# Optimization experiments

Measured on AMD Instinct MI355X. Metric: run time of the kernel, lower is better.

## Reference

```python
import jax, jax.numpy as jnp
import numpy as np
import math

B, L, E, H, FF = 8, 1024, 1024, 16, 4096
DH = E // H  # 64
EPS = 1e-10


def layer_norm(x, gamma, beta):
    mean = jnp.mean(x, axis=-1, keepdims=True)
    var = jnp.mean((x - mean) ** 2, axis=-1, keepdims=True)
    return gamma * (x - mean) / jnp.sqrt(var + EPS) + beta


def setup_inputs() -> dict:
    key = jax.random.key(0)
    ks = jax.random.split(key, 16)
    c_qk = math.sqrt(6.0 / (E + DH))
    c_o = math.sqrt(6.0 / (H * DH + E))
    c1 = math.sqrt(6.0 / (E + FF))
    c2 = math.sqrt(6.0 / (FF + E))
    u = lambda k, shp, c: jax.random.uniform(k, shp, jnp.float32, -c, c)
    return {
        "x": jax.random.normal(ks[0], (B, L, E), jnp.float32),
        # per-head projections stacked: [H, E, DH] (stored input-major = W^T of torch Linear)
        "Wq": u(ks[1], (H, E, DH), c_qk), "bq": jnp.zeros((H, DH), jnp.float32),
        "Wk": u(ks[2], (H, E, DH), c_qk), "bk": jnp.zeros((H, DH), jnp.float32),
        "Wv": u(ks[3], (H, E, DH), c_qk), "bv": jnp.zeros((H, DH), jnp.float32),
        "Wo": u(ks[4], (H * DH, E), c_o), "bo": jnp.zeros((E,), jnp.float32),
        "W1": u(ks[5], (E, FF), c1), "b1": jnp.zeros((FF,), jnp.float32),
        "W2": u(ks[6], (FF, E), c2), "b2": jnp.zeros((E,), jnp.float32),
        "gamma1": jnp.ones((E,), jnp.float32), "beta1": jnp.zeros((E,), jnp.float32),
        "gamma2": jnp.ones((E,), jnp.float32), "beta2": jnp.zeros((E,), jnp.float32),
    }


def reference(x, Wq, bq, Wk, bk, Wv, bv, Wo, bo, W1, b1, W2, b2, gamma1, beta1, gamma2, beta2):
    # multi-head attention (all heads batched; concat order == head order)
    q = jnp.einsum("ble,hed->bhld", x, Wq) + bq[None, :, None, :]
    k = jnp.einsum("ble,hed->bhld", x, Wk) + bk[None, :, None, :]
    v = jnp.einsum("ble,hed->bhld", x, Wv) + bv[None, :, None, :]
    scores = jnp.einsum("bhld,bhmd->bhlm", q, k) / math.sqrt(DH)
    weights = jax.nn.softmax(scores, axis=-1)
    y = jnp.einsum("bhlm,bhmd->bhld", weights, v)          # [B,H,L,DH]
    concat = y.transpose(0, 2, 1, 3).reshape(B, L, H * DH)  # [B,L,E]
    out1 = concat @ Wo + bo
    # residual + LN (dropout p=0 -> identity)
    out2 = layer_norm(out1 + x, gamma1, beta1)
    # FFN
    out3 = jax.nn.relu(out2 @ W1 + b1) @ W2 + b2
    return layer_norm(out3 + out2, gamma2, beta2)
```

## Files before the change

### kernel.cpp

```cpp
#include <hip/hip_runtime.h>
#include <hip/hip_bf16.h>

#define BB 8
#define LL 1024
#define EE 1024
#define HH 16
#define DHH 64
#define FFF 4096

typedef __attribute__((ext_vector_type(8))) short short8;
typedef __attribute__((ext_vector_type(4))) float f32x4;

__device__ inline f32x4 mfma16(short8 a, short8 b, f32x4 c) {
    return __builtin_amdgcn_mfma_f32_16x16x32_bf16(a, b, c, 0, 0, 0);
}

__device__ inline void async_ld16(const __hip_bfloat16* g, __hip_bfloat16* l) {
    __builtin_amdgcn_global_load_lds(
        (const __attribute__((address_space(1))) void*)g,
        (__attribute__((address_space(3))) void*)l, 16, 0, 0);
}

__device__ inline unsigned short bf16bits(float f) {
    __hip_bfloat16 h = __float2bfloat16(f);
    return *reinterpret_cast<unsigned short*>(&h);
}

__device__ inline float bf2f(unsigned short u) {
    unsigned v = ((unsigned)u) << 16;
    return *reinterpret_cast<float*>(&v);
}

__device__ inline float exp2_fast(float x) {
    float r;
    asm("v_exp_f32 %0, %1" : "=v"(r) : "v"(x));
    return r;
}

__device__ inline unsigned cvt_pk_bf16(float lo, float hi) {
    unsigned r;
    asm("v_cvt_pk_bf16_f32 %0, %1, %2" : "=v"(r) : "v"(lo), "v"(hi));
    return r;
}

__device__ inline void wg_barrier() {
    __builtin_amdgcn_sched_barrier(0);
    asm volatile("" ::: "memory");
    __builtin_amdgcn_s_barrier();
    asm volatile("" ::: "memory");
    __builtin_amdgcn_sched_barrier(0);
}

__global__ __launch_bounds__(256) void wtrans_all(
    const float* __restrict__ Wq, const float* __restrict__ Wk, const float* __restrict__ Wv,
    const float* __restrict__ Wo, const float* __restrict__ W1, const float* __restrict__ W2,
    const float* __restrict__ x,
    __hip_bfloat16* __restrict__ wqkvt, __hip_bfloat16* __restrict__ wot,
    __hip_bfloat16* __restrict__ w1t, __hip_bfloat16* __restrict__ w2t,
    __hip_bfloat16* __restrict__ xb) {
    const int id = blockIdx.x;
    const int tid = threadIdx.x;
    if (id >= 3072) {
        const int xi = id - 3072;
#pragma unroll
        for (int j = 0; j < 4; ++j) {
            const size_t f4 = (size_t)xi * 1024 + j * 256 + tid;
            float4 v = reinterpret_cast<const float4*>(x)[f4];
            ushort4 o;
            o.x = bf16bits(v.x); o.y = bf16bits(v.y); o.z = bf16bits(v.z); o.w = bf16bits(v.w);
            reinterpret_cast<ushort4*>(xb)[f4] = o;
        }
        return;
    }
    const float* src;
    __hip_bfloat16* dst;
    int K, N, k0, n0;
    if (id < 768) {
        const int which = id >> 8, r = id & 255;
        const int z = r >> 4, xx = r & 15;
        src = ((which == 0) ? Wq : (which == 1) ? Wk : Wv) + (size_t)z * 65536;
        dst = wqkvt + (size_t)which * 1024 * 1024 + (size_t)z * 65536;
        K = 1024; N = 64; k0 = xx * 64; n0 = 0;
    } else if (id < 1024) {
        const int r = id - 768;
        src = Wo; dst = wot; K = 1024; N = 1024; k0 = (r & 15) * 64; n0 = (r >> 4) * 64;
    } else if (id < 2048) {
        const int r = id - 1024;
        src = W1; dst = w1t; K = 1024; N = 4096; k0 = (r & 15) * 64; n0 = (r >> 4) * 64;
    } else {
        const int r = id - 2048;
        src = W2; dst = w2t; K = 4096; N = 1024; k0 = (r & 63) * 64; n0 = (r >> 6) * 64;
    }
    __shared__ __hip_bfloat16 t[64 * 66];
#pragma unroll
    for (int i = 0; i < 16; ++i) {
        int idx = tid + i * 256;
        int kr = idx >> 6, nc = idx & 63;
        t[kr * 66 + nc] = __float2bfloat16(src[(size_t)(k0 + kr) * N + n0 + nc]);
    }
    __syncthreads();
#pragma unroll
    for (int i = 0; i < 16; ++i) {
        int idx = tid + i * 256;
        int nr = idx >> 6, kc = idx & 63;
        dst[(size_t)(n0 + nr) * K + k0 + kc] = t[kc * 66 + nr];
    }
}

template <int MODE, int CM, int CN, int ZX>
__global__ __launch_bounds__(512, 2) void gemm256(
    const __hip_bfloat16* __restrict__ A, const __hip_bfloat16* __restrict__ Bm,
    int M, int N, int K, int ksplit, size_t zstride, void* __restrict__ Cout,
    const float* __restrict__ bias0, const float* __restrict__ bias1,
    const float* __restrict__ bias2, __hip_bfloat16* __restrict__ vtout) {
    __shared__ __hip_bfloat16 lds[2][2][2][128 * 64];
    const int flat = blockIdx.x + gridDim.x * (blockIdx.y + gridDim.y * blockIdx.z);
    const int xcd = flat & 7, rank = flat >> 3;
    const int mc = xcd & 3, hc = xcd >> 2;
    const int ml = rank / CN, nl = rank % CN;
    const int mb = mc * CM + ml;
    const int nb = ZX ? nl : (hc * CN + nl);
    const int zb = ZX ? hc : 0;
    const int m0 = mb * 256, n0 = nb * 256;
    const int tid = threadIdx.x;
    const int wid = tid >> 6, l = tid & 63;
    const int wm = wid >> 2, wn = wid & 3;
    const int lr = l & 15, lg = l >> 4;
    const int T = K / (64 * ksplit);
    const int kb = zb * T;

    const int c0 = tid, c1 = tid + 512;
    const int r0 = c0 >> 3, s0 = (((c0 & 7) ^ (r0 & 7)) << 3);
    const int r1 = c1 >> 3, s1 = (((c1 & 7) ^ (r1 & 7)) << 3);
    const int ldst0 = wid * 512;
    const int ldst1 = 4096 + wid * 512;

#define STAGE(bi, isb, half, kt)                                                             \
    do {                                                                                     \
        const __hip_bfloat16* _s = (isb) ? Bm : A;                                           \
        const int _br = ((isb) ? n0 : m0) + (half) * 128;                                    \
        __hip_bfloat16* _d = &lds[bi][isb][half][0];                                         \
        async_ld16(_s + (size_t)(_br + r0) * K + (size_t)(kb + (kt)) * 64 + s0, _d + ldst0); \
        async_ld16(_s + (size_t)(_br + r1) * K + (size_t)(kb + (kt)) * 64 + s1, _d + ldst1); \
    } while (0)

    f32x4 acc[8][4];
#pragma unroll
    for (int m = 0; m < 8; ++m)
#pragma unroll
        for (int n = 0; n < 4; ++n) acc[m][n] = (f32x4){0.f, 0.f, 0.f, 0.f};

    short8 aLo[4][2], aHi[4][2], bR[4][2];

#define LDA(dst, bi, m, kh)                                                          \
    do {                                                                             \
        const int _ra = (m) * 16 + lr;                                               \
        const int _sl = ((kh) * 4 + lg) ^ (_ra & 7);                                 \
        dst = *reinterpret_cast<const short8*>(&lds[bi][0][wm][_ra * 64 + _sl * 8]); \
    } while (0)
#define LDB(dst, bi, n, kh)                                                               \
    do {                                                                                  \
        const int _rb = (wn & 1) * 64 + (n) * 16 + lr;                                    \
        const int _sl = ((kh) * 4 + lg) ^ (_rb & 7);                                      \
        dst = *reinterpret_cast<const short8*>(&lds[bi][1][wn >> 1][_rb * 64 + _sl * 8]); \
    } while (0)

#define RD_ALO(bi)                      \
    _Pragma("unroll") for (int m = 0; m < 4; ++m) { \
        LDA(aLo[m][0], bi, m, 0);       \
        LDA(aLo[m][1], bi, m, 1);       \
    }
#define RD_AHI(bi)                      \
    _Pragma("unroll") for (int m = 0; m < 4; ++m) { \
        LDA(aHi[m][0], bi, m + 4, 0);   \
        LDA(aHi[m][1], bi, m + 4, 1);   \
    }
#define RD_B01(bi)                      \
    _Pragma("unroll") for (int n = 0; n < 2; ++n) { \
        LDB(bR[n][0], bi, n, 0);        \
        LDB(bR[n][1], bi, n, 1);        \
    }
#define RD_B23(bi)                      \
    _Pragma("unroll") for (int n = 2; n < 4; ++n) { \
        LDB(bR[n][0], bi, n, 0);        \
        LDB(bR[n][1], bi, n, 1);        \
    }
#define MFMA_Q(mbase, afr, nlo)                                            \
    __builtin_amdgcn_s_setprio(1);                                         \
    _Pragma("unroll") for (int m = 0; m < 4; ++m) {                        \
        _Pragma("unroll") for (int n = (nlo); n < (nlo) + 2; ++n) {        \
            acc[(mbase) + m][n] = mfma16(afr[m][0], bR[n][0], acc[(mbase) + m][n]); \
            acc[(mbase) + m][n] = mfma16(afr[m][1], bR[n][1], acc[(mbase) + m][n]); \
        }                                                                  \
    }                                                                      \
    __builtin_amdgcn_s_setprio(0);

    STAGE(0, 1, 0, 0);
    STAGE(0, 1, 1, 0);
    STAGE(0, 0, 0, 0);
    STAGE(0, 0, 1, 0);
    if (T > 1) {
        STAGE(1, 1, 0, 1);
        STAGE(1, 1, 1, 1);
        STAGE(1, 0, 0, 1);
        STAGE(1, 0, 1, 1);
        asm volatile("s_waitcnt vmcnt(8)" ::: "memory");
    } else {
        asm volatile("s_waitcnt vmcnt(0)" ::: "memory");
    }
    wg_barrier();
    RD_ALO(0);
    RD_B01(0);

    for (int t = 0; t < T; ++t) {
        const int cur = t & 1, nxt = cur ^ 1;
        wg_barrier();
        MFMA_Q(0, aLo, 0);
        RD_B23(cur);
        wg_barrier();
        MFMA_Q(0, aLo, 2);
        RD_AHI(cur);
        if (t + 2 < T) STAGE(cur, 1, 0, t + 2);
        wg_barrier();
        MFMA_Q(4, aHi, 0);
        if (t + 2 < T) {
            asm volatile("s_waitcnt vmcnt(2)" ::: "memory");
            STAGE(cur, 1, 1, t + 2);
            STAGE(cur, 0, 0, t + 2);
            STAGE(cur, 0, 1, t + 2);
        } else if (t + 1 < T) {
            asm volatile("s_waitcnt vmcnt(0)" ::: "memory");
        }
        wg_barrier();
        MFMA_Q(4, aHi, 2);
        if (t + 1 < T) {
            RD_ALO(nxt);
            RD_B01(nxt);
        }
    }
#undef STAGE
#undef LDA
#undef LDB
#undef RD_ALO
#undef RD_AHI
#undef RD_B01
#undef RD_B23
#undef MFMA_Q

    asm volatile("s_waitcnt vmcnt(0)" ::: "memory");
    __syncthreads();

    float* eb = reinterpret_cast<float*>(&lds[0][0][0][0]) + wid * (16 * 68);
    const int erow = l >> 3, ec = l & 7;
    const int rowg = m0 + wm * 128;
    const int colg = n0 + wn * 64;
    float bv[4];
#pragma unroll
    for (int n = 0; n < 4; ++n) {
        if constexpr (MODE == 0) {
            const int col = colg + n * 16 + lr;
            int s = col >> 10;
            const float* bp = (s == 0) ? bias0 : ((s == 1) ? bias1 : bias2);
            bv[n] = bp[col & 1023];
        } else if constexpr (MODE == 2) {
            bv[n] = bias0[colg + n * 16 + lr];
        } else {
            bv[n] = 0.f;
        }
    }
    __hip_bfloat16* Cb = (MODE == 4)
        ? ((__hip_bfloat16*)Cout + (size_t)zb * zstride)
        : (__hip_bfloat16*)Cout;
#pragma unroll
    for (int m = 0; m < 8; ++m) {
#pragma unroll
        for (int n = 0; n < 4; ++n)
#pragma unroll
            for (int r = 0; r < 4; ++r) {
                float v = acc[m][n][r] + bv[n];
                if constexpr (MODE == 2) v = fmaxf(v, 0.f);
                eb[(lg * 4 + r) * 68 + n * 16 + lr] = v;
            }
#pragma unroll
        for (int i = 0; i < 2; ++i) {
            const int rr = erow + i * 8;
            float4 v0 = *reinterpret_cast<float4*>(&eb[rr * 68 + ec * 8]);
            float4 v1 = *reinterpret_cast<float4*>(&eb[rr * 68 + ec * 8 + 4]);
            uint4 o;
            o.x = cvt_pk_bf16(v0.x, v0.y);
            o.y = cvt_pk_bf16(v0.z, v0.w);
            o.z = cvt_pk_bf16(v1.x, v1.y);
            o.w = cvt_pk_bf16(v1.z, v1.w);
            *reinterpret_cast<uint4*>(&Cb[(size_t)(rowg + m * 16 + rr) * N + colg + ec * 8]) = o;
        }
        if constexpr (MODE == 0) {
            if (colg >= 2048) {
                const int h2 = (colg - 2048) >> 6;
                const int bh2 = ((rowg >> 10) << 4) + h2;
                const int l0 = (rowg & 1023) + m * 16;
                uint4 o0, o1;
                o0.x = cvt_pk_bf16(eb[0 * 68 + l], eb[1 * 68 + l]);
                o0.y = cvt_pk_bf16(eb[2 * 68 + l], eb[3 * 68 + l]);
                o0.z = cvt_pk_bf16(eb[4 * 68 + l], eb[5 * 68 + l]);
                o0.w = cvt_pk_bf16(eb[6 * 68 + l], eb[7 * 68 + l]);
                o1.x = cvt_pk_bf16(eb[8 * 68 + l], eb[9 * 68 + l]);
                o1.y = cvt_pk_bf16(eb[10 * 68 + l], eb[11 * 68 + l]);
                o1.z = cvt_pk_bf16(eb[12 * 68 + l], eb[13 * 68 + l]);
                o1.w = cvt_pk_bf16(eb[14 * 68 + l], eb[15 * 68 + l]);
                __hip_bfloat16* vrow = vtout + ((size_t)bh2 * 64 + l) * 1024 + l0;
                *reinterpret_cast<uint4*>(vrow) = o0;
                *reinterpret_cast<uint4*>(vrow + 8) = o1;
            }
        }
    }
}

__global__ __launch_bounds__(512, 4) void attn4(const __hip_bfloat16* __restrict__ qkv,
                                                const __hip_bfloat16* __restrict__ vt,
                                                __hip_bfloat16* __restrict__ cat) {
    const int orig = blockIdx.y * 4 + blockIdx.x;
    const int swz = (orig & 7) * 64 + (orig >> 3);
    const int qt = swz & 3, bh = swz >> 2;
    const int b = bh >> 4, h = bh & 15;
    const int tid = threadIdx.x, w = tid >> 6, l = tid & 63;
    const int lr = l & 15, lg = l >> 4;
    const int sw = lr & 7;

    __shared__ __hip_bfloat16 Ks[2][64 * 64];
    __shared__ __hip_bfloat16 Vs[2][64 * 64];
    __shared__ __hip_bfloat16 plds[8][32 * 72];

    short8 qa[2][2];
#pragma unroll
    for (int q = 0; q < 2; ++q) {
        const size_t qrow = (size_t)(b * LL + qt * 256 + w * 32 + q * 16 + lr);
        qa[q][0] = *reinterpret_cast<const short8*>(qkv + qrow * 3072 + h * 64 + lg * 8);
        qa[q][1] = *reinterpret_cast<const short8*>(qkv + qrow * 3072 + h * 64 + 32 + lg * 8);
    }

    const int rA = tid >> 3, sA = (((tid & 7) ^ (rA & 7)) << 3);
    const __hip_bfloat16* kg = qkv + (size_t)(b * LL + rA) * 3072 + 1024 + h * 64 + sA;
    const __hip_bfloat16* vg = vt + ((size_t)bh * 64 + rA) * LL + sA;

#define STAGE_KV(bi, k0)                                        \
    do {                                                        \
        async_ld16(kg + (size_t)(k0) * 3072, &Ks[bi][w * 512]); \
        async_ld16(vg + (k0), &Vs[bi][w * 512]);                \
    } while (0)

    float mrun[2] = {-INFINITY, -INFINITY}, lrun[2] = {0.f, 0.f};
    f32x4 oacc[2][4];
#pragma unroll
    for (int q = 0; q < 2; ++q)
#pragma unroll
        for (int n = 0; n < 4; ++n) oacc[q][n] = (f32x4){0.f, 0.f, 0.f, 0.f};

    STAGE_KV(0, 0);
    asm volatile("s_waitcnt vmcnt(0)" ::: "memory");
    __syncthreads();

    const float SCALE = 0.18033688011112042f;

    int cur = 0;
    for (int kt = 0; kt < 16; ++kt) {
        if (kt < 15) STAGE_KV(cur ^ 1, (kt + 1) * 64);

        f32x4 s[2][4];
#pragma unroll
        for (int m = 0; m < 4; ++m) {
            const int krow = m * 16 + lr;
            const short8 kf0 =
                *reinterpret_cast<const short8*>(&Ks[cur][krow * 64 + ((lg ^ sw) << 3)]);
            const short8 kf1 =
                *reinterpret_cast<const short8*>(&Ks[cur][krow * 64 + (((lg + 4) ^ sw) << 3)]);
#pragma unroll
            for (int q = 0; q < 2; ++q) {
                f32x4 t = (f32x4){0.f, 0.f, 0.f, 0.f};
                t = mfma16(kf0, qa[q][0], t);
                t = mfma16(kf1, qa[q][1], t);
                s[q][m] = t * SCALE;
            }
        }
        float smax[2];
#pragma unroll
        for (int q = 0; q < 2; ++q) {
            float mx = s[q][0][0];
#pragma unroll
            for (int m = 0; m < 4; ++m)
#pragma unroll
                for (int r = 0; r < 4; ++r) mx = fmaxf(mx, s[q][m][r]);
            mx = fmaxf(mx, __shfl_xor(mx, 16, 64));
            mx = fmaxf(mx, __shfl_xor(mx, 32, 64));
            smax[q] = mx;
        }
        if (__any(fmaxf(smax[0] - mrun[0], smax[1] - mrun[1]) > 8.0f)) {
#pragma unroll
            for (int q = 0; q < 2; ++q) {
                const float mnew = fmaxf(mrun[q], smax[q]);
                const float alpha = exp2_fast(mrun[q] - mnew);
                mrun[q] = mnew;
                lrun[q] *= alpha;
#pragma unroll
                for (int r = 0; r < 4; ++r) {
                    const float aD = __shfl(alpha, lg * 4 + r, 64);
#pragma unroll
                    for (int n = 0; n < 4; ++n) oacc[q][n][r] *= aD;
                }
            }
        }
#pragma unroll
        for (int q = 0; q < 2; ++q) {
            float tsum = 0.f;
#pragma unroll
            for (int m = 0; m < 4; ++m) {
                float p0 = exp2_fast(s[q][m][0] - mrun[q]);
                float p1 = exp2_fast(s[q][m][1] - mrun[q]);
                float p2 = exp2_fast(s[q][m][2] - mrun[q]);
                float p3 = exp2_fast(s[q][m][3] - mrun[q]);
                tsum += (p0 + p1) + (p2 + p3);
                uint2 d;
                d.x = cvt_pk_bf16(p0, p1);
                d.y = cvt_pk_bf16(p2, p3);
                *reinterpret_cast<uint2*>(&plds[w][(q * 16 + lr) * 72 + m * 16 + lg * 4]) = d;
            }
            tsum += __shfl_xor(tsum, 16, 64);
            tsum += __shfl_xor(tsum, 32, 64);
            lrun[q] += tsum;
        }
        asm volatile("s_waitcnt lgkmcnt(0)" ::: "memory");
        __builtin_amdgcn_sched_barrier(0);

        short8 pa[2][2];
#pragma unroll
        for (int q = 0; q < 2; ++q) {
            pa[q][0] = *reinterpret_cast<const short8*>(&plds[w][(q * 16 + lr) * 72 + lg * 8]);
            pa[q][1] =
                *reinterpret_cast<const short8*>(&plds[w][(q * 16 + lr) * 72 + 32 + lg * 8]);
        }
#pragma unroll
        for (int n = 0; n < 4; ++n) {
            const int vrow = n * 16 + lr;
            const short8 vf0 =
                *reinterpret_cast<const short8*>(&Vs[cur][vrow * 64 + ((lg ^ sw) << 3)]);
            const short8 vf1 =
                *reinterpret_cast<const short8*>(&Vs[cur][vrow * 64 + (((lg + 4) ^ sw) << 3)]);
#pragma unroll
            for (int q = 0; q < 2; ++q) {
                oacc[q][n] = mfma16(pa[q][0], vf0, oacc[q][n]);
                oacc[q][n] = mfma16(pa[q][1], vf1, oacc[q][n]);
            }
        }

        asm volatile("s_waitcnt vmcnt(0)" ::: "memory");
        __syncthreads();
        cur ^= 1;
    }
#undef STAGE_KV

#pragma unroll
    for (int q = 0; q < 2; ++q) {
        float rinv[4];
#pragma unroll
        for (int r = 0; r < 4; ++r) rinv[r] = 1.0f / __shfl(lrun[q], lg * 4 + r, 64);
#pragma unroll
        for (int n = 0; n < 4; ++n)
#pragma unroll
            for (int r = 0; r < 4; ++r) {
                const float v = oacc[q][n][r] * rinv[r];
                cat[(size_t)(b * LL + qt * 256 + w * 32 + q * 16 + lg * 4 + r) * EE + h * 64 +
                    n * 16 + lr] = __float2bfloat16(v);
            }
    }
}

template <bool CBF16, bool OUTF32>
__global__ __launch_bounds__(256) void ln_fused(const __hip_bfloat16* __restrict__ a,
                                                const __hip_bfloat16* __restrict__ b,
                                                const void* __restrict__ cv,
                                                const float* __restrict__ colbias,
                                                const float* __restrict__ gamma,
                                                const float* __restrict__ beta,
                                                void* __restrict__ outv) {
    const int row = blockIdx.x, tid = threadIdx.x;
    const size_t base = (size_t)row * EE;
    const ushort4 ua = reinterpret_cast<const ushort4*>(a + base)[tid];
    const ushort4 ub = reinterpret_cast<const ushort4*>(b + base)[tid];
    float4 z;
    if constexpr (CBF16) {
        const ushort4 uc =
            reinterpret_cast<const ushort4*>((const __hip_bfloat16*)cv + base)[tid];
        z.x = bf2f(uc.x); z.y = bf2f(uc.y); z.z = bf2f(uc.z); z.w = bf2f(uc.w);
    } else {
        z = reinterpret_cast<const float4*>((const float*)cv + base)[tid];
    }
    float4 cb = reinterpret_cast<const float4*>(colbias)[tid];
    float4 x;
    x.x = bf2f(ua.x) + bf2f(ub.x) + z.x + cb.x;
    x.y = bf2f(ua.y) + bf2f(ub.y) + z.y + cb.y;
    x.z = bf2f(ua.z) + bf2f(ub.z) + z.z + cb.z;
    x.w = bf2f(ua.w) + bf2f(ub.w) + z.w + cb.w;
    float s = x.x + x.y + x.z + x.w;
    float s2 = x.x * x.x + x.y * x.y + x.z * x.z + x.w * x.w;
#pragma unroll
    for (int msk = 1; msk < 64; msk <<= 1) {
        s += __shfl_xor(s, msk, 64);
        s2 += __shfl_xor(s2, msk, 64);
    }
    __shared__ float red[8];
    const int w = tid >> 6, l = tid & 63;
    if (l == 0) { red[w] = s; red[4 + w] = s2; }
    __syncthreads();
    s = red[0] + red[1] + red[2] + red[3];
    s2 = red[4] + red[5] + red[6] + red[7];
    const float mean = s * (1.f / 1024.f);
    const float var = s2 * (1.f / 1024.f) - mean * mean;
    const float rstd = rsqrtf(var + 1e-10f);
    float4 g = reinterpret_cast<const float4*>(gamma)[tid];
    float4 bt = reinterpret_cast<const float4*>(beta)[tid];
    float4 o;
    o.x = g.x * (x.x - mean) * rstd + bt.x;
    o.y = g.y * (x.y - mean) * rstd + bt.y;
    o.z = g.z * (x.z - mean) * rstd + bt.z;
    o.w = g.w * (x.w - mean) * rstd + bt.w;
    if constexpr (OUTF32) {
        reinterpret_cast<float4*>((float*)outv + base)[tid] = o;
    } else {
        ushort4 ob;
        ob.x = bf16bits(o.x); ob.y = bf16bits(o.y); ob.z = bf16bits(o.z); ob.w = bf16bits(o.w);
        reinterpret_cast<ushort4*>((__hip_bfloat16*)outv + base)[tid] = ob;
    }
}

extern "C" void kernel_launch(void* const* d_in, const int* in_sizes, int n_in,
                              void* d_out, int out_size, void* d_ws, size_t ws_size,
                              hipStream_t stream) {
    const float* x = (const float*)d_in[0];
    const float* Wq = (const float*)d_in[1];
    const float* bq = (const float*)d_in[2];
    const float* Wk = (const float*)d_in[3];
    const float* bk = (const float*)d_in[4];
    const float* Wv = (const float*)d_in[5];
    const float* bv = (const float*)d_in[6];
    const float* Wo = (const float*)d_in[7];
    const float* bo = (const float*)d_in[8];
    const float* W1 = (const float*)d_in[9];
    const float* b1 = (const float*)d_in[10];
    const float* W2 = (const float*)d_in[11];
    const float* b2 = (const float*)d_in[12];
    const float* gamma1 = (const float*)d_in[13];
    const float* beta1 = (const float*)d_in[14];
    const float* gamma2 = (const float*)d_in[15];
    const float* beta2 = (const float*)d_in[16];
    float* out = (float*)d_out;

    char* Wb = (char*)d_ws;
    const size_t MB = (size_t)1 << 20;
    if (ws_size < 168 * MB) return;
    __hip_bfloat16* xb = (__hip_bfloat16*)(Wb + 0 * MB);
    __hip_bfloat16* wqkvt = (__hip_bfloat16*)(Wb + 16 * MB);
    __hip_bfloat16* wot = (__hip_bfloat16*)(Wb + 22 * MB);
    __hip_bfloat16* w1t = (__hip_bfloat16*)(Wb + 24 * MB);
    __hip_bfloat16* w2t = (__hip_bfloat16*)(Wb + 32 * MB);
    __hip_bfloat16* qkvb = (__hip_bfloat16*)(Wb + 40 * MB);
    __hip_bfloat16* vtb = (__hip_bfloat16*)(Wb + 88 * MB);
    __hip_bfloat16* catb = (__hip_bfloat16*)(Wb + 104 * MB);
    __hip_bfloat16* p0 = (__hip_bfloat16*)(Wb + 40 * MB);
    __hip_bfloat16* out2b = (__hip_bfloat16*)(Wb + 136 * MB);
    __hip_bfloat16* hbuf = (__hip_bfloat16*)(Wb + 40 * MB);
    __hip_bfloat16* q0 = (__hip_bfloat16*)(Wb + 0 * MB);
    const size_t PSTRIDE = (size_t)8192 * 1024;

    wtrans_all<<<5120, 256, 0, stream>>>(Wq, Wk, Wv, Wo, W1, W2, x, wqkvt, wot, w1t, w2t, xb);
    gemm256<0, 8, 6, 0><<<dim3(32, 12, 1), 512, 0, stream>>>(xb, wqkvt, 8192, 3072, 1024, 1, 0,
                                                             qkvb, bq, bk, bv, vtb);
    attn4<<<dim3(4, 128), 512, 0, stream>>>(qkvb, vtb, catb);
    gemm256<4, 8, 4, 1><<<dim3(32, 4, 2), 512, 0, stream>>>(catb, wot, 8192, 1024, 1024, 2,
                                                            PSTRIDE, p0, nullptr, nullptr,
                                                            nullptr, nullptr);
    ln_fused<false, false><<<8192, 256, 0, stream>>>(p0, p0 + PSTRIDE, x, bo, gamma1, beta1,
                                                     out2b);
    gemm256<2, 8, 8, 0><<<dim3(32, 16, 1), 512, 0, stream>>>(out2b, w1t, 8192, 4096, 1024, 1, 0,
                                                             hbuf, b1, nullptr, nullptr,
                                                             nullptr);
    gemm256<4, 8, 4, 1><<<dim3(32, 4, 2), 512, 0, stream>>>(hbuf, w2t, 8192, 1024, 4096, 2,
                                                            PSTRIDE, q0, nullptr, nullptr,
                                                            nullptr, nullptr);
    ln_fused<true, true><<<8192, 256, 0, stream>>>(q0, q0 + PSTRIDE, out2b, b2, gamma2, beta2,
                                                   out);
}
```

Measured before the change: 301.5 us.

## Halve GEMM k-tile to 32 and use 4-way split-K for Wo and W2 projections

The GEMM k-step drops from 64 to 32, which halves LDS use per block and simplifies the pipeline to two barriers per iteration with a new swizzled layout. The Wo and W2 GEMMs switch from 2-way to 4-way split-K, giving 512 blocks instead of 256 to fill the CUs. The layer-norm kernels now sum four bf16 partials. The cost is more partial-buffer traffic, more barriers per unit of K, and extra bf16 rounding from summing four partials.

```diff
diff --git a/kernel.cpp b/kernel.cpp
--- a/kernel.cpp
+++ b/kernel.cpp
@@ -107,41 +107,44 @@
     }
 }
 
-template <int MODE, int CM, int CN, int ZX>
+template <int MODE, int CM, int CN, int NZ>
 __global__ __launch_bounds__(512, 2) void gemm256(
     const __hip_bfloat16* __restrict__ A, const __hip_bfloat16* __restrict__ Bm,
-    int M, int N, int K, int ksplit, size_t zstride, void* __restrict__ Cout,
+    int M, int N, int K, size_t zstride, size_t z2off, void* __restrict__ Cout,
     const float* __restrict__ bias0, const float* __restrict__ bias1,
     const float* __restrict__ bias2, __hip_bfloat16* __restrict__ vtout) {
-    __shared__ __hip_bfloat16 lds[2][2][2][128 * 64];
+    __shared__ __hip_bfloat16 lds[2][2][2][64 * 64];
     const int flat = blockIdx.x + gridDim.x * (blockIdx.y + gridDim.y * blockIdx.z);
     const int xcd = flat & 7, rank = flat >> 3;
-    const int mc = xcd & 3, hc = xcd >> 2;
-    const int ml = rank / CN, nl = rank % CN;
-    const int mb = mc * CM + ml;
-    const int nb = ZX ? nl : (hc * CN + nl);
-    const int zb = ZX ? hc : 0;
+    int mb, nb, zb;
+    if constexpr (NZ == 1) {
+        mb = (xcd & 3) * CM + rank / CN;
+        nb = (xcd >> 2) * CN + rank % CN;
+        zb = 0;
+    } else {
+        mb = xcd * CM + rank / (CN * NZ);
+        const int rem = rank % (CN * NZ);
+        zb = rem / CN;
+        nb = rem % CN;
+    }
     const int m0 = mb * 256, n0 = nb * 256;
     const int tid = threadIdx.x;
     const int wid = tid >> 6, l = tid & 63;
     const int wm = wid >> 2, wn = wid & 3;
     const int lr = l & 15, lg = l >> 4;
-    const int T = K / (64 * ksplit);
+    const int T = K / (32 * NZ);
     const int kb = zb * T;
 
-    const int c0 = tid, c1 = tid + 512;
-    const int r0 = c0 >> 3, s0 = (((c0 & 7) ^ (r0 & 7)) << 3);
-    const int r1 = c1 >> 3, s1 = (((c1 & 7) ^ (r1 & 7)) << 3);
-    const int ldst0 = wid * 512;
-    const int ldst1 = 4096 + wid * 512;
-
-#define STAGE(bi, isb, half, kt)                                                             \
-    do {                                                                                     \
-        const __hip_bfloat16* _s = (isb) ? Bm : A;                                           \
-        const int _br = ((isb) ? n0 : m0) + (half) * 128;                                    \
-        __hip_bfloat16* _d = &lds[bi][isb][half][0];                                         \
-        async_ld16(_s + (size_t)(_br + r0) * K + (size_t)(kb + (kt)) * 64 + s0, _d + ldst0); \
-        async_ld16(_s + (size_t)(_br + r1) * K + (size_t)(kb + (kt)) * 64 + s1, _d + ldst1); \
+    const int p_ = tid >> 3, c_ = tid & 7, u_ = c_ ^ (p_ & 7);
+    const int srow = 2 * p_ + (u_ >> 2);
+    const int skc = (u_ & 3) << 3;
+
+#define STAGE(bi, isb, half, kt)                                                     \
+    do {                                                                             \
+        const __hip_bfloat16* _s = (isb) ? Bm : A;                                   \
+        const int _br = ((isb) ? n0 : m0) + (half) * 128;                            \
+        async_ld16(_s + (size_t)(_br + srow) * K + (size_t)(kb + (kt)) * 32 + skc,   \
+                   &lds[bi][isb][half][0] + wid * 512);                              \
     } while (0)
 
     f32x4 acc[8][4];
@@ -150,92 +153,70 @@
 #pragma unroll
         for (int n = 0; n < 4; ++n) acc[m][n] = (f32x4){0.f, 0.f, 0.f, 0.f};
 
-    short8 aLo[4][2], aHi[4][2], bR[4][2];
-
-#define LDA(dst, bi, m, kh)                                                          \
+    short8 aLo[4], aHi[4], bR[4];
+
+#define LDA(dst, bi, m)                                                              \
     do {                                                                             \
-        const int _ra = (m) * 16 + lr;                                               \
-        const int _sl = ((kh) * 4 + lg) ^ (_ra & 7);                                 \
-        dst = *reinterpret_cast<const short8*>(&lds[bi][0][wm][_ra * 64 + _sl * 8]); \
+        const int _r = (m) * 16 + lr;                                                \
+        const int _p = _r >> 1;                                                      \
+        const int _c = (lg + ((_r & 1) << 2)) ^ (_p & 7);                            \
+        dst = *reinterpret_cast<const short8*>(&lds[bi][0][wm][_p * 64 + _c * 8]);   \
     } while (0)
-#define LDB(dst, bi, n, kh)                                                               \
-    do {                                                                                  \
-        const int _rb = (wn & 1) * 64 + (n) * 16 + lr;                                    \
-        const int _sl = ((kh) * 4 + lg) ^ (_rb & 7);                                      \
-        dst = *reinterpret_cast<const short8*>(&lds[bi][1][wn >> 1][_rb * 64 + _sl * 8]); \
+#define LDB(dst, bi, n)                                                              \
+    do {                                                                             \
+        const int _r = (wn & 1) * 64 + (n) * 16 + lr;                                \
+        const int _p = _r >> 1;                                                      \
+        const int _c = (lg + ((_r & 1) << 2)) ^ (_p & 7);                            \
+        dst = *reinterpret_cast<const short8*>(&lds[bi][1][wn >> 1][_p * 64 + _c * 8]); \
     } while (0)
 
-#define RD_ALO(bi)                      \
-    _Pragma("unroll") for (int m = 0; m < 4; ++m) { \
-        LDA(aLo[m][0], bi, m, 0);       \
-        LDA(aLo[m][1], bi, m, 1);       \
-    }
-#define RD_AHI(bi)                      \
-    _Pragma("unroll") for (int m = 0; m < 4; ++m) { \
-        LDA(aHi[m][0], bi, m + 4, 0);   \
-        LDA(aHi[m][1], bi, m + 4, 1);   \
-    }
-#define RD_B01(bi)                      \
-    _Pragma("unroll") for (int n = 0; n < 2; ++n) { \
-        LDB(bR[n][0], bi, n, 0);        \
-        LDB(bR[n][1], bi, n, 1);        \
-    }
-#define RD_B23(bi)                      \
-    _Pragma("unroll") for (int n = 2; n < 4; ++n) { \
-        LDB(bR[n][0], bi, n, 0);        \
-        LDB(bR[n][1], bi, n, 1);        \
-    }
-#define MFMA_Q(mbase, afr, nlo)                                            \
-    __builtin_amdgcn_s_setprio(1);                                         \
-    _Pragma("unroll") for (int m = 0; m < 4; ++m) {                        \
-        _Pragma("unroll") for (int n = (nlo); n < (nlo) + 2; ++n) {        \
-            acc[(mbase) + m][n] = mfma16(afr[m][0], bR[n][0], acc[(mbase) + m][n]); \
-            acc[(mbase) + m][n] = mfma16(afr[m][1], bR[n][1], acc[(mbase) + m][n]); \
-        }                                                                  \
-    }                                                                      \
+#define RD_ALO(bi) \
+    _Pragma("unroll") for (int m = 0; m < 4; ++m) LDA(aLo[m], bi, m);
+#define RD_AHI(bi) \
+    _Pragma("unroll") for (int m = 0; m < 4; ++m) LDA(aHi[m], bi, m + 4);
+#define RD_B(bi) \
+    _Pragma("unroll") for (int n = 0; n < 4; ++n) LDB(bR[n], bi, n);
+#define MFMA_Q(mbase, afr)                                                           \
+    __builtin_amdgcn_s_setprio(1);                                                   \
+    _Pragma("unroll") for (int m = 0; m < 4; ++m) {                                  \
+        _Pragma("unroll") for (int n = 0; n < 4; ++n) {                              \
+            acc[(mbase) + m][n] = mfma16(afr[m], bR[n], acc[(mbase) + m][n]);        \
+        }                                                                            \
+    }                                                                                \
     __builtin_amdgcn_s_setprio(0);
 
     STAGE(0, 1, 0, 0);
     STAGE(0, 1, 1, 0);
     STAGE(0, 0, 0, 0);
     STAGE(0, 0, 1, 0);
-    if (T > 1) {
-        STAGE(1, 1, 0, 1);
-        STAGE(1, 1, 1, 1);
-        STAGE(1, 0, 0, 1);
-        STAGE(1, 0, 1, 1);
-        asm volatile("s_waitcnt vmcnt(8)" ::: "memory");
-    } else {
-        asm volatile("s_waitcnt vmcnt(0)" ::: "memory");
-    }
+    STAGE(1, 1, 0, 1);
+    STAGE(1, 1, 1, 1);
+    STAGE(1, 0, 0, 1);
+    STAGE(1, 0, 1, 1);
+    asm volatile("s_waitcnt vmcnt(4)" ::: "memory");
     wg_barrier();
     RD_ALO(0);
-    RD_B01(0);
+    RD_B(0);
 
     for (int t = 0; t < T; ++t) {
         const int cur = t & 1, nxt = cur ^ 1;
+        MFMA_Q(0, aLo);
+        RD_AHI(cur);
         wg_barrier();
-        MFMA_Q(0, aLo, 0);
-        RD_B23(cur);
-        wg_barrier();
-        MFMA_Q(0, aLo, 2);
-        RD_AHI(cur);
-        if (t + 2 < T) STAGE(cur, 1, 0, t + 2);
-        wg_barrier();
-        MFMA_Q(4, aHi, 0);
+        MFMA_Q(4, aHi);
         if (t + 2 < T) {
-            asm volatile("s_waitcnt vmcnt(2)" ::: "memory");
+            STAGE(cur, 1, 0, t + 2);
             STAGE(cur, 1, 1, t + 2);
             STAGE(cur, 0, 0, t + 2);
             STAGE(cur, 0, 1, t + 2);
+            asm volatile("s_waitcnt vmcnt(4)" ::: "memory");
         } else if (t + 1 < T) {
             asm volatile("s_waitcnt vmcnt(0)" ::: "memory");
         }
         wg_barrier();
-        MFMA_Q(4, aHi, 2);
         if (t + 1 < T) {
             RD_ALO(nxt);
-            RD_B01(nxt);
+            RD_B(nxt);
         }
     }
 #undef STAGE
@@ -243,8 +224,7 @@
 #undef LDB
 #undef RD_ALO
 #undef RD_AHI
-#undef RD_B01
-#undef RD_B23
+#undef RD_B
 #undef MFMA_Q
 
     asm volatile("s_waitcnt vmcnt(0)" ::: "memory");
@@ -268,9 +248,11 @@
             bv[n] = 0.f;
         }
     }
-    __hip_bfloat16* Cb = (MODE == 4)
-        ? ((__hip_bfloat16*)Cout + (size_t)zb * zstride)
-        : (__hip_bfloat16*)Cout;
+    __hip_bfloat16* Cb = (__hip_bfloat16*)Cout;
+    if constexpr (MODE == 4) {
+        Cb += (size_t)(zb & 1) * zstride;
+        if (zb >= 2) Cb += z2off;
+    }
 #pragma unroll
     for (int m = 0; m < 8; ++m) {
 #pragma unroll
@@ -474,17 +456,21 @@
 }
 
 template <bool CBF16, bool OUTF32>
-__global__ __launch_bounds__(256) void ln_fused(const __hip_bfloat16* __restrict__ a,
-                                                const __hip_bfloat16* __restrict__ b,
-                                                const void* __restrict__ cv,
-                                                const float* __restrict__ colbias,
-                                                const float* __restrict__ gamma,
-                                                const float* __restrict__ beta,
-                                                void* __restrict__ outv) {
+__global__ __launch_bounds__(256) void ln_fused4(const __hip_bfloat16* __restrict__ a0,
+                                                 const __hip_bfloat16* __restrict__ a1,
+                                                 const __hip_bfloat16* __restrict__ a2,
+                                                 const __hip_bfloat16* __restrict__ a3,
+                                                 const void* __restrict__ cv,
+                                                 const float* __restrict__ colbias,
+                                                 const float* __restrict__ gamma,
+                                                 const float* __restrict__ beta,
+                                                 void* __restrict__ outv) {
     const int row = blockIdx.x, tid = threadIdx.x;
     const size_t base = (size_t)row * EE;
-    const ushort4 ua = reinterpret_cast<const ushort4*>(a + base)[tid];
-    const ushort4 ub = reinterpret_cast<const ushort4*>(b + base)[tid];
+    const ushort4 u0 = reinterpret_cast<const ushort4*>(a0 + base)[tid];
+    const ushort4 u1 = reinterpret_cast<const ushort4*>(a1 + base)[tid];
+    const ushort4 u2 = reinterpret_cast<const ushort4*>(a2 + base)[tid];
+    const ushort4 u3 = reinterpret_cast<const ushort4*>(a3 + base)[tid];
     float4 z;
     if constexpr (CBF16) {
         const ushort4 uc =
@@ -495,10 +481,10 @@
     }
     float4 cb = reinterpret_cast<const float4*>(colbias)[tid];
     float4 x;
-    x.x = bf2f(ua.x) + bf2f(ub.x) + z.x + cb.x;
-    x.y = bf2f(ua.y) + bf2f(ub.y) + z.y + cb.y;
-    x.z = bf2f(ua.z) + bf2f(ub.z) + z.z + cb.z;
-    x.w = bf2f(ua.w) + bf2f(ub.w) + z.w + cb.w;
+    x.x = (bf2f(u0.x) + bf2f(u1.x)) + (bf2f(u2.x) + bf2f(u3.x)) + z.x + cb.x;
+    x.y = (bf2f(u0.y) + bf2f(u1.y)) + (bf2f(u2.y) + bf2f(u3.y)) + z.y + cb.y;
+    x.z = (bf2f(u0.z) + bf2f(u1.z)) + (bf2f(u2.z) + bf2f(u3.z)) + z.z + cb.z;
+    x.w = (bf2f(u0.w) + bf2f(u1.w)) + (bf2f(u2.w) + bf2f(u3.w)) + z.w + cb.w;
     float s = x.x + x.y + x.z + x.w;
     float s2 = x.x * x.x + x.y * x.y + x.z * x.z + x.w * x.w;
 #pragma unroll
@@ -568,23 +554,24 @@
     __hip_bfloat16* out2b = (__hip_bfloat16*)(Wb + 136 * MB);
     __hip_bfloat16* hbuf = (__hip_bfloat16*)(Wb + 40 * MB);
     __hip_bfloat16* q0 = (__hip_bfloat16*)(Wb + 0 * MB);
+    __hip_bfloat16* q2 = (__hip_bfloat16*)(Wb + 104 * MB);
     const size_t PSTRIDE = (size_t)8192 * 1024;
+    const size_t Q2OFF = (size_t)104 * MB / 2;
 
     wtrans_all<<<5120, 256, 0, stream>>>(Wq, Wk, Wv, Wo, W1, W2, x, wqkvt, wot, w1t, w2t, xb);
-    gemm256<0, 8, 6, 0><<<dim3(32, 12, 1), 512, 0, stream>>>(xb, wqkvt, 8192, 3072, 1024, 1, 0,
-                                                             qkvb, bq, bk, bv, vtb);
+    gemm256<0, 8, 6, 1><<<dim3(32, 12, 1), 512, 0, stream>>>(
+        xb, wqkvt, 8192, 3072, 1024, 0, 0, qkvb, bq, bk, bv, vtb);
     attn4<<<dim3(4, 128), 512, 0, stream>>>(qkvb, vtb, catb);
-    gemm256<4, 8, 4, 1><<<dim3(32, 4, 2), 512, 0, stream>>>(catb, wot, 8192, 1024, 1024, 2,
-                                                            PSTRIDE, p0, nullptr, nullptr,
-                                                            nullptr, nullptr);
-    ln_fused<false, false><<<8192, 256, 0, stream>>>(p0, p0 + PSTRIDE, x, bo, gamma1, beta1,
-                                                     out2b);
-    gemm256<2, 8, 8, 0><<<dim3(32, 16, 1), 512, 0, stream>>>(out2b, w1t, 8192, 4096, 1024, 1, 0,
-                                                             hbuf, b1, nullptr, nullptr,
-                                                             nullptr);
-    gemm256<4, 8, 4, 1><<<dim3(32, 4, 2), 512, 0, stream>>>(hbuf, w2t, 8192, 1024, 4096, 2,
-                                                            PSTRIDE, q0, nullptr, nullptr,
-                                                            nullptr, nullptr);
-    ln_fused<true, true><<<8192, 256, 0, stream>>>(q0, q0 + PSTRIDE, out2b, b2, gamma2, beta2,
-                                                   out);
-}
+    gemm256<4, 4, 4, 4><<<dim3(32, 4, 4), 512, 0, stream>>>(
+        catb, wot, 8192, 1024, 1024, PSTRIDE, 2 * PSTRIDE, p0, nullptr, nullptr, nullptr,
+        nullptr);
+    ln_fused4<false, false><<<8192, 256, 0, stream>>>(p0, p0 + PSTRIDE, p0 + 2 * PSTRIDE,
+                                                      p0 + 3 * PSTRIDE, x, bo, gamma1, beta1,
+                                                      out2b);
+    gemm256<2, 8, 8, 1><<<dim3(32, 16, 1), 512, 0, stream>>>(
+        out2b, w1t, 8192, 4096, 1024, 0, 0, hbuf, b1, nullptr, nullptr, nullptr);
+    gemm256<4, 4, 4, 4><<<dim3(32, 4, 4), 512, 0, stream>>>(
+        hbuf, w2t, 8192, 1024, 4096, PSTRIDE, Q2OFF, q0, nullptr, nullptr, nullptr, nullptr);
+    ln_fused4<true, true><<<8192, 256, 0, stream>>>(q0, q0 + PSTRIDE, q2, q2 + PSTRIDE, out2b,
+                                                    b2, gamma2, beta2, out);
+}
```

New measurement: 335.9 us. +11.4%, slower.
